# Performance work log

Measured on AMD Instinct MI355X. Metric: run time of the kernel, lower is better.

Reference implementation:

```python
import jax, jax.numpy as jnp
import numpy as np

O, I = 4096, 4096          # out_features, in_features
N = 8192                   # tokens (batch*seq)
ROW_BS, COL_BS = 1, 4      # block sparsity granularity
ZP_OUT = 0                 # output zero point (int)
QMIN, QMAX = -128.0, 127.0 # qint8 range


def setup_inputs() -> dict:
    key = jax.random.key(0)
    k1, k2, k3, k4 = jax.random.split(key, 4)
    # dequantized fp32 activations
    x = jax.random.normal(k1, (N, I), dtype=jnp.float32)
    # int8 weight values (zero point 0), stored as float32 integers in [-127,127]
    w_q = jnp.round(jnp.clip(jax.random.normal(k2, (O, I), dtype=jnp.float32) * 40.0, QMIN + 1, QMAX))
    bias = jax.random.normal(k3, (O,), dtype=jnp.float32) * 0.1
    block_mask = jax.random.randint(k4, (O // ROW_BS, I // COL_BS), 0, 2, dtype=jnp.int32)
    w_scale = jnp.float32(0.01)   # per-tensor weight scale, weight zp == 0
    out_scale = jnp.float32(0.05) # activation (output) quant scale
    return {"x": x, "w_q": w_q, "bias": bias, "w_scale": w_scale,
            "out_scale": out_scale, "block_mask": block_mask}


def reference(x, w_q, bias, w_scale, out_scale, block_mask):
    # expand block mask to element mask [O, I]
    m = jnp.repeat(jnp.repeat(block_mask, ROW_BS, axis=0), COL_BS, axis=1).astype(w_q.dtype)
    w_eff = w_q * m                                  # masked int8 weight values
    # dequantized GEMM: (x @ W^T) * w_scale + bias
    y = jnp.einsum('ni,oi->no', x, w_eff) * w_scale + bias  # [N, O]
    # quantize output to qint8 (scale=out_scale, zp=ZP_OUT), return dequantized repr
    q = jnp.clip(jnp.round(y / out_scale) + ZP_OUT, QMIN, QMAX)
    return (q - ZP_OUT) * out_scale
```

## Files before the change

### kernel.cpp

```cpp
#include <hip/hip_runtime.h>


#define M_TOK 8192
#define O_FEAT 4096
#define K_FEAT 4096

#define BM 256
#define BN 256
#define BK 64
#define NT (K_FEAT / BK)

using f16x8 = __attribute__((ext_vector_type(8))) _Float16;
using f32x4 = __attribute__((ext_vector_type(4))) float;

#define BAR()    asm volatile("s_barrier" ::: "memory")
#define LGKM0()  asm volatile("s_waitcnt lgkmcnt(0)" ::: "memory")
#define VMCNT(n) asm volatile("s_waitcnt vmcnt(" #n ")" ::: "memory")
#define MFMA16(a, b, c) __builtin_amdgcn_mfma_f32_16x16x32_f16((a), (b), (c), 0, 0, 0)

__global__ __launch_bounds__(256) void cvt_x_kernel(const float* __restrict__ x,
                                                    _Float16* __restrict__ xf) {
    size_t i = ((size_t)blockIdx.x * 256 + threadIdx.x) * 8;
    float4 v0 = *reinterpret_cast<const float4*>(x + i);
    float4 v1 = *reinterpret_cast<const float4*>(x + i + 4);
    f16x8 h;
    h[0] = (_Float16)v0.x; h[1] = (_Float16)v0.y;
    h[2] = (_Float16)v0.z; h[3] = (_Float16)v0.w;
    h[4] = (_Float16)v1.x; h[5] = (_Float16)v1.y;
    h[6] = (_Float16)v1.z; h[7] = (_Float16)v1.w;
    *reinterpret_cast<f16x8*>(xf + i) = h;
}

__global__ __launch_bounds__(256) void cvt_w_kernel(const float* __restrict__ wq,
                                                    const int* __restrict__ mask,
                                                    _Float16* __restrict__ wf) {
    size_t i = ((size_t)blockIdx.x * 256 + threadIdx.x) * 8;
    float4 v0 = *reinterpret_cast<const float4*>(wq + i);
    float4 v1 = *reinterpret_cast<const float4*>(wq + i + 4);
    int2 mv = *reinterpret_cast<const int2*>(mask + i / 4);
    float m0 = mv.x ? 1.0f : 0.0f;
    float m1 = mv.y ? 1.0f : 0.0f;
    f16x8 h;
    h[0] = (_Float16)(v0.x * m0); h[1] = (_Float16)(v0.y * m0);
    h[2] = (_Float16)(v0.z * m0); h[3] = (_Float16)(v0.w * m0);
    h[4] = (_Float16)(v1.x * m1); h[5] = (_Float16)(v1.y * m1);
    h[6] = (_Float16)(v1.z * m1); h[7] = (_Float16)(v1.w * m1);
    *reinterpret_cast<f16x8*>(wf + i) = h;
}

__global__ __launch_bounds__(512, 2) void gemm_kernel(const _Float16* __restrict__ A,
                                                      const _Float16* __restrict__ B,
                                                      const float* __restrict__ bias,
                                                      const float* __restrict__ wsp,
                                                      const float* __restrict__ osp,
                                                      float* __restrict__ C) {
    __shared__ __align__(16) _Float16 smem[2][2][2][BM * 32];

    const int tid  = threadIdx.x;
    const int lane = tid & 63;
    const int w    = tid >> 6;
    const int wm   = w >> 2;
    const int wn   = w & 3;
    const int lr   = lane & 15;
    const int kq   = lane >> 4;

    const int bm = blockIdx.x >> 4;
    const int bn = blockIdx.x & 15;

    const _Float16* Abase = A + (size_t)(bm * BM) * K_FEAT;
    const _Float16* Bbase = B + (size_t)(bn * BN) * K_FEAT;

    const int sr0  = w * 32 + (lane >> 2);
    const int csrc = (((lane & 3) ^ ((lane >> 3) & 3))) * 8;

    auto stage = [&](int buf, int mat, int kh, const _Float16* gbase, int t) {
#pragma unroll
        for (int j = 0; j < 2; ++j) {
            const int r = sr0 + j * 16;
            const _Float16* src = gbase + (size_t)r * K_FEAT + t * BK + kh * 32 + csrc;
            _Float16* dst = &smem[buf][mat][kh][(w * 128 + j * 64 + lane) * 8];
            __builtin_amdgcn_global_load_lds(
                (const __attribute__((address_space(1))) void*)(const void*)src,
                (__attribute__((address_space(3))) void*)(void*)dst, 16, 0, 0);
        }
    };
    auto lda = [&](int buf, int kh, int m) -> f16x8 {
        const int r = wm * 128 + m * 16 + lr;
        return *reinterpret_cast<const f16x8*>(
            &smem[buf][0][kh][r * 32 + ((kq ^ ((r >> 1) & 3)) << 3)]);
    };
    auto ldb = [&](int buf, int kh, int n) -> f16x8 {
        const int r = wn * 64 + n * 16 + lr;
        return *reinterpret_cast<const f16x8*>(
            &smem[buf][1][kh][r * 32 + ((kq ^ ((r >> 1) & 3)) << 3)]);
    };

    f32x4 acc[8][4] = {};
    f16x8 a[8], bf[4];

    stage(0, 0, 0, Abase, 0);
    stage(0, 1, 0, Bbase, 0);
    stage(0, 0, 1, Abase, 0);
    stage(0, 1, 1, Bbase, 0);
    stage(1, 0, 0, Abase, 1);
    VMCNT(6);
    BAR();

    for (int s = 0; s < NT; ++s) {
        const int b = s & 1;

        if (s + 1 < NT) stage(b ^ 1, 1, 0, Bbase, s + 1);
#pragma unroll
        for (int m = 0; m < 8; ++m) a[m] = lda(b, 0, m);
        bf[0] = ldb(b, 0, 0);
        bf[1] = ldb(b, 0, 1);
        BAR();
        LGKM0();
        __builtin_amdgcn_s_setprio(1);
#pragma unroll
        for (int m = 0; m < 8; ++m) {
            acc[m][0] = MFMA16(a[m], bf[0], acc[m][0]);
            acc[m][1] = MFMA16(a[m], bf[1], acc[m][1]);
        }
        __builtin_amdgcn_s_setprio(0);
        BAR();

        if (s + 1 < NT) stage(b ^ 1, 0, 1, Abase, s + 1);
        bf[2] = ldb(b, 0, 2);
        bf[3] = ldb(b, 0, 3);
        BAR();
        LGKM0();
        __builtin_amdgcn_s_setprio(1);
#pragma unroll
        for (int m = 0; m < 8; ++m) {
            acc[m][2] = MFMA16(a[m], bf[2], acc[m][2]);
            acc[m][3] = MFMA16(a[m], bf[3], acc[m][3]);
        }
        __builtin_amdgcn_s_setprio(0);
        if (s == NT - 1) { VMCNT(0); } else { VMCNT(6); }
        BAR();

        if (s + 1 < NT) stage(b ^ 1, 1, 1, Bbase, s + 1);
#pragma unroll
        for (int m = 0; m < 8; ++m) a[m] = lda(b, 1, m);
        bf[0] = ldb(b, 1, 0);
        bf[1] = ldb(b, 1, 1);
        BAR();
        LGKM0();
        __builtin_amdgcn_s_setprio(1);
#pragma unroll
        for (int m = 0; m < 8; ++m) {
            acc[m][0] = MFMA16(a[m], bf[0], acc[m][0]);
            acc[m][1] = MFMA16(a[m], bf[1], acc[m][1]);
        }
        __builtin_amdgcn_s_setprio(0);
        BAR();

        if (s + 2 < NT) stage(b, 0, 0, Abase, s + 2);
        bf[2] = ldb(b, 1, 2);
        bf[3] = ldb(b, 1, 3);
        BAR();
        LGKM0();
        __builtin_amdgcn_s_setprio(1);
#pragma unroll
        for (int m = 0; m < 8; ++m) {
            acc[m][2] = MFMA16(a[m], bf[2], acc[m][2]);
            acc[m][3] = MFMA16(a[m], bf[3], acc[m][3]);
        }
        __builtin_amdgcn_s_setprio(0);
        if (s == NT - 2)      { VMCNT(4); }
        else if (s < NT - 2)  { VMCNT(6); }
        BAR();
    }

    const float wscale = wsp[0];
    const float oscale = osp[0];
    const int row0 = bm * BM + wm * 128;
    const int col0 = bn * BN + wn * 64;
#pragma unroll
    for (int n = 0; n < 4; ++n) {
        const int col = col0 + n * 16 + lr;
        const float bc = bias[col];
#pragma unroll
        for (int m = 0; m < 8; ++m) {
#pragma unroll
            for (int j = 0; j < 4; ++j) {
                const int row = row0 + m * 16 + kq * 4 + j;
                float y = acc[m][n][j] * wscale + bc;
                float q = rintf(y / oscale);
                q = fminf(fmaxf(q, -128.0f), 127.0f);
                C[(size_t)row * O_FEAT + col] = q * oscale;
            }
        }
    }
}

extern "C" void kernel_launch(void* const* d_in, const int* in_sizes, int n_in,
                              void* d_out, int out_size, void* d_ws, size_t ws_size,
                              hipStream_t stream) {
    const float* x        = (const float*)d_in[0];
    const float* wq       = (const float*)d_in[1];
    const float* bias     = (const float*)d_in[2];
    const float* w_scale  = (const float*)d_in[3];
    const float* out_scale= (const float*)d_in[4];
    const int*   mask     = (const int*)d_in[5];
    float* out = (float*)d_out;

    _Float16* xf = (_Float16*)d_ws;
    _Float16* wf = (_Float16*)((char*)d_ws + (size_t)M_TOK * K_FEAT * 2);

    cvt_x_kernel<<<(M_TOK * (size_t)K_FEAT) / 8 / 256, 256, 0, stream>>>(x, xf);
    cvt_w_kernel<<<(O_FEAT * (size_t)K_FEAT) / 8 / 256, 256, 0, stream>>>(wq, mask, wf);

    gemm_kernel<<<dim3((M_TOK / BM) * (O_FEAT / BN)), 512, 0, stream>>>(
        xf, wf, bias, w_scale, out_scale, out);
}
```

Baseline: 309.1 us.

## Restructure GEMM main loop into 4x4 MFMA sub-tiles with register double-buffering

Reworks the GEMM k-loop so each phase issues a 4x4 block of MFMAs from register fragments loaded in the previous phase, splitting A into two halves and B into two k-half fragments. The explicit lgkmcnt(0) waits go away, so LDS reads for the next phase overlap with the current MFMA work, and the global-to-LDS staging is rescheduled with a shallower prefetch depth. The aim is to hide LDS latency behind matrix math and raise MFMA issue density. The cost is a tighter hazard schedule: LDS reads now rely on compiler-inserted waits, and the shallower global prefetch may expose memory latency.

New measurement: 300.2 us. 2.9% less time.

```diff
diff --git a/kernel.cpp b/kernel.cpp
--- a/kernel.cpp
+++ b/kernel.cpp
@@ -14,7 +14,6 @@
 using f32x4 = __attribute__((ext_vector_type(4))) float;
 
 #define BAR()    asm volatile("s_barrier" ::: "memory")
-#define LGKM0()  asm volatile("s_waitcnt lgkmcnt(0)" ::: "memory")
 #define VMCNT(n) asm volatile("s_waitcnt vmcnt(" #n ")" ::: "memory")
 #define MFMA16(a, b, c) __builtin_amdgcn_mfma_f32_16x16x32_f16((a), (b), (c), 0, 0, 0)
 
@@ -96,81 +95,79 @@
     };
 
     f32x4 acc[8][4] = {};
-    f16x8 a[8], bf[4];
+    f16x8 a0[4], a1[4], b0[4], b1[4];
 
     stage(0, 0, 0, Abase, 0);
     stage(0, 1, 0, Bbase, 0);
+    VMCNT(0);
+    BAR();
+#pragma unroll
+    for (int m = 0; m < 4; ++m) a0[m] = lda(0, 0, m);
+#pragma unroll
+    for (int n = 0; n < 4; ++n) b0[n] = ldb(0, 0, n);
     stage(0, 0, 1, Abase, 0);
     stage(0, 1, 1, Bbase, 0);
-    stage(1, 0, 0, Abase, 1);
-    VMCNT(6);
-    BAR();
 
     for (int s = 0; s < NT; ++s) {
-        const int b = s & 1;
-
-        if (s + 1 < NT) stage(b ^ 1, 1, 0, Bbase, s + 1);
-#pragma unroll
-        for (int m = 0; m < 8; ++m) a[m] = lda(b, 0, m);
-        bf[0] = ldb(b, 0, 0);
-        bf[1] = ldb(b, 0, 1);
-        BAR();
-        LGKM0();
-        __builtin_amdgcn_s_setprio(1);
-#pragma unroll
-        for (int m = 0; m < 8; ++m) {
-            acc[m][0] = MFMA16(a[m], bf[0], acc[m][0]);
-            acc[m][1] = MFMA16(a[m], bf[1], acc[m][1]);
+        const int b  = s & 1;
+        const int nb = b ^ 1;
+
+#pragma unroll
+        for (int m = 0; m < 4; ++m) a1[m] = lda(b, 0, 4 + m);
+        if (s + 1 < NT) stage(nb, 0, 0, Abase, s + 1);
+        BAR();
+        __builtin_amdgcn_s_setprio(1);
+#pragma unroll
+        for (int m = 0; m < 4; ++m)
+#pragma unroll
+            for (int n = 0; n < 4; ++n)
+                acc[m][n] = MFMA16(a0[m], b0[n], acc[m][n]);
+        __builtin_amdgcn_s_setprio(0);
+        if (s == NT - 1) { VMCNT(0); } else { VMCNT(2); }
+        BAR();
+
+#pragma unroll
+        for (int m = 0; m < 4; ++m) a0[m] = lda(b, 1, m);
+#pragma unroll
+        for (int n = 0; n < 4; ++n) b1[n] = ldb(b, 1, n);
+        if (s + 1 < NT) stage(nb, 1, 0, Bbase, s + 1);
+        BAR();
+        __builtin_amdgcn_s_setprio(1);
+#pragma unroll
+        for (int m = 0; m < 4; ++m)
+#pragma unroll
+            for (int n = 0; n < 4; ++n)
+                acc[4 + m][n] = MFMA16(a1[m], b0[n], acc[4 + m][n]);
+        __builtin_amdgcn_s_setprio(0);
+
+#pragma unroll
+        for (int m = 0; m < 4; ++m) a1[m] = lda(b, 1, 4 + m);
+        if (s + 1 < NT) stage(nb, 0, 1, Abase, s + 1);
+        BAR();
+        __builtin_amdgcn_s_setprio(1);
+#pragma unroll
+        for (int m = 0; m < 4; ++m)
+#pragma unroll
+            for (int n = 0; n < 4; ++n)
+                acc[m][n] = MFMA16(a0[m], b1[n], acc[m][n]);
+        __builtin_amdgcn_s_setprio(0);
+        if (s + 1 < NT) { VMCNT(2); BAR(); }
+
+        if (s + 1 < NT) {
+#pragma unroll
+            for (int m = 0; m < 4; ++m) a0[m] = lda(nb, 0, m);
+#pragma unroll
+            for (int n = 0; n < 4; ++n) b0[n] = ldb(nb, 0, n);
+            stage(nb, 1, 1, Bbase, s + 1);
         }
-        __builtin_amdgcn_s_setprio(0);
-        BAR();
-
-        if (s + 1 < NT) stage(b ^ 1, 0, 1, Abase, s + 1);
-        bf[2] = ldb(b, 0, 2);
-        bf[3] = ldb(b, 0, 3);
-        BAR();
-        LGKM0();
-        __builtin_amdgcn_s_setprio(1);
-#pragma unroll
-        for (int m = 0; m < 8; ++m) {
-            acc[m][2] = MFMA16(a[m], bf[2], acc[m][2]);
-            acc[m][3] = MFMA16(a[m], bf[3], acc[m][3]);
-        }
-        __builtin_amdgcn_s_setprio(0);
-        if (s == NT - 1) { VMCNT(0); } else { VMCNT(6); }
-        BAR();
-
-        if (s + 1 < NT) stage(b ^ 1, 1, 1, Bbase, s + 1);
-#pragma unroll
-        for (int m = 0; m < 8; ++m) a[m] = lda(b, 1, m);
-        bf[0] = ldb(b, 1, 0);
-        bf[1] = ldb(b, 1, 1);
-        BAR();
-        LGKM0();
-        __builtin_amdgcn_s_setprio(1);
-#pragma unroll
-        for (int m = 0; m < 8; ++m) {
-            acc[m][0] = MFMA16(a[m], bf[0], acc[m][0]);
-            acc[m][1] = MFMA16(a[m], bf[1], acc[m][1]);
-        }
-        __builtin_amdgcn_s_setprio(0);
-        BAR();
-
-        if (s + 2 < NT) stage(b, 0, 0, Abase, s + 2);
-        bf[2] = ldb(b, 1, 2);
-        bf[3] = ldb(b, 1, 3);
-        BAR();
-        LGKM0();
-        __builtin_amdgcn_s_setprio(1);
-#pragma unroll
-        for (int m = 0; m < 8; ++m) {
-            acc[m][2] = MFMA16(a[m], bf[2], acc[m][2]);
-            acc[m][3] = MFMA16(a[m], bf[3], acc[m][3]);
-        }
-        __builtin_amdgcn_s_setprio(0);
-        if (s == NT - 2)      { VMCNT(4); }
-        else if (s < NT - 2)  { VMCNT(6); }
-        BAR();
+        BAR();
+        __builtin_amdgcn_s_setprio(1);
+#pragma unroll
+        for (int m = 0; m < 4; ++m)
+#pragma unroll
+            for (int n = 0; n < 4; ++n)
+                acc[4 + m][n] = MFMA16(a1[m], b1[n], acc[4 + m][n]);
+        __builtin_amdgcn_s_setprio(0);
     }
 
     const float wscale = wsp[0];
```
